# Kernel optimization log

Hardware: AMD Instinct MI355X
Metric: run time of the kernel (lower is better)

The kernel has to match this reference:

```python
import jax
import jax.numpy as jnp
import numpy as np

B, S, D, H, HID, E, TOPK = 1, 2048, 1024, 16, 4096, 8, 2
HEAD_DIM = D // H


def _layer_norm(x, g, b, eps=1e-5):
    mu = jnp.mean(x, axis=-1, keepdims=True)
    var = jnp.var(x, axis=-1, keepdims=True)
    return (x - mu) * jax.lax.rsqrt(var + eps) * g + b


def setup_inputs() -> dict:
    key = jax.random.key(0)
    ks = jax.random.split(key, 12)
    s = 0.02
    return {
        "x": jax.random.normal(ks[0], (B, S, D), jnp.float32),
        "ln1_g": jnp.ones((D,), jnp.float32),
        "ln1_b": jnp.zeros((D,), jnp.float32),
        "wq": jax.random.normal(ks[1], (D, D), jnp.float32) * s,
        "wk": jax.random.normal(ks[2], (D, D), jnp.float32) * s,
        "wv": jax.random.normal(ks[3], (D, D), jnp.float32) * s,
        "wo": jax.random.normal(ks[4], (D, D), jnp.float32) * s,
        "ln2_g": jnp.ones((D,), jnp.float32),
        "ln2_b": jnp.zeros((D,), jnp.float32),
        "w_gate": jax.random.normal(ks[5], (D, E), jnp.float32) * s,
        "w_eg": jax.random.normal(ks[6], (E, D, HID), jnp.float32) * s,
        "w_eu": jax.random.normal(ks[7], (E, D, HID), jnp.float32) * s,
        "w_ed": jax.random.normal(ks[8], (E, HID, D), jnp.float32) * s,
    }


def _attention(h, wq, wk, wv, wo):
    b, s, d = h.shape
    q = (h @ wq).reshape(b, s, H, HEAD_DIM).transpose(0, 2, 1, 3)
    k = (h @ wk).reshape(b, s, H, HEAD_DIM).transpose(0, 2, 1, 3)
    v = (h @ wv).reshape(b, s, H, HEAD_DIM).transpose(0, 2, 1, 3)
    scores = jnp.einsum("bhqd,bhkd->bhqk", q, k) / jnp.sqrt(jnp.asarray(HEAD_DIM, h.dtype))
    causal = jnp.tril(jnp.ones((s, s), bool))  # [s,s]
    scores = jnp.where(causal, scores, jnp.asarray(-1e30, h.dtype))
    attn = jax.nn.softmax(scores, axis=-1)
    out = jnp.einsum("bhqk,bhkd->bhqd", attn, v).transpose(0, 2, 1, 3).reshape(b, s, d)
    return out @ wo


def _moe(h, w_gate, w_eg, w_eu, w_ed):
    b, s, d = h.shape
    flat = h.reshape(-1, d)  # [T,D]
    logits = flat @ w_gate  # [T,E]
    scores = jax.nn.sigmoid(logits)
    top_val, top_idx = jax.lax.top_k(scores, TOPK)
    top_val = top_val / (jnp.sum(top_val, axis=-1, keepdims=True) + 1e-9)
    # per-token per-expert combine weight (0 for unrouted experts)
    combine = jnp.sum(jax.nn.one_hot(top_idx, E, dtype=flat.dtype) * top_val[..., None], axis=1)  # [T,E]
    g = jax.nn.silu(jnp.einsum("td,edh->eth", flat, w_eg))
    u = jnp.einsum("td,edh->eth", flat, w_eu)
    eo = jnp.einsum("eth,ehd->etd", g * u, w_ed)  # [E,T,D]
    out = jnp.einsum("etd,te->td", eo, combine)
    return out.reshape(b, s, d)


def reference(x, ln1_g, ln1_b, wq, wk, wv, wo, ln2_g, ln2_b, w_gate, w_eg, w_eu, w_ed):
    x = x + _attention(_layer_norm(x, ln1_g, ln1_b), wq, wk, wv, wo)
    x = x + _moe(_layer_norm(x, ln2_g, ln2_b), w_gate, w_eg, w_eu, w_ed)
    return x
```

## Files before the change

kernel.cpp:

```cpp
#include <hip/hip_runtime.h>
#include <hip/hip_bf16.h>
#include <stdint.h>

#define DI __device__ __forceinline__

typedef short bf16x8_t __attribute__((ext_vector_type(8)));
typedef float f32x4_t __attribute__((ext_vector_type(4)));

DI unsigned short f2bf(float f) {
  __hip_bfloat16 h = __float2bfloat16(f);
  unsigned short u;
  __builtin_memcpy(&u, &h, 2);
  return u;
}

DI uint32_t pk2(float a, float b) {
  return (uint32_t)f2bf(a) | ((uint32_t)f2bf(b) << 16);
}

DI f32x4_t mfma16(bf16x8_t a, bf16x8_t b, f32x4_t c) {
  return __builtin_amdgcn_mfma_f32_16x16x32_bf16(a, b, c, 0, 0, 0);
}

DI void gload16(const void* g, void* l) {
  __builtin_amdgcn_global_load_lds(
      (const __attribute__((address_space(1))) uint32_t*)g,
      (__attribute__((address_space(3))) uint32_t*)l, 16, 0, 0);
}

DI bf16x8_t frag(const unsigned short* base, int row, int hi) {
  return *(const bf16x8_t*)&base[row * 32 + ((hi ^ ((row >> 1) & 3)) * 8)];
}
DI int chunk_swz(int tid) { return ((tid & 3) ^ ((tid >> 3) & 3)) * 8; }

__global__ __launch_bounds__(256) void transpose_cvt(const float* __restrict__ in,
                                                     unsigned short* __restrict__ out,
                                                     int R, int C) {
  __shared__ float tile[64][65];
  const int tid = threadIdx.x;
  const int tx = tid & 15, ty = tid >> 4;
  const size_t zoff = (size_t)blockIdx.z * R * C;
  const int r0 = blockIdx.y * 64, c0 = blockIdx.x * 64;
#pragma unroll
  for (int i = 0; i < 4; ++i) {
    const int r = ty + i * 16;
    const float4 v = *(const float4*)(in + zoff + (size_t)(r0 + r) * C + c0 + tx * 4);
    tile[r][tx * 4 + 0] = v.x; tile[r][tx * 4 + 1] = v.y;
    tile[r][tx * 4 + 2] = v.z; tile[r][tx * 4 + 3] = v.w;
  }
  __syncthreads();
#pragma unroll
  for (int i = 0; i < 4; ++i) {
    const int r = ty + i * 16;
    ushort4 o;
    o.x = f2bf(tile[tx * 4 + 0][r]); o.y = f2bf(tile[tx * 4 + 1][r]);
    o.z = f2bf(tile[tx * 4 + 2][r]); o.w = f2bf(tile[tx * 4 + 3][r]);
    *(ushort4*)(out + zoff + (size_t)(c0 + r) * R + r0 + tx * 4) = o;
  }
}

__global__ __launch_bounds__(256) void ln_kernel(const float* __restrict__ x, const float* __restrict__ g,
                                                 const float* __restrict__ b, unsigned short* __restrict__ out) {
  const int row = blockIdx.x, tid = threadIdx.x;
  const int wid = tid >> 6, lane = tid & 63;
  const float4 v = *(const float4*)(x + (size_t)row * 1024 + tid * 4);
  float s = v.x + v.y + v.z + v.w;
  float s2 = v.x * v.x + v.y * v.y + v.z * v.z + v.w * v.w;
#pragma unroll
  for (int o = 1; o < 64; o <<= 1) { s += __shfl_xor(s, o); s2 += __shfl_xor(s2, o); }
  __shared__ float red[8];
  if (lane == 0) { red[wid] = s; red[4 + wid] = s2; }
  __syncthreads();
  const float ts = red[0] + red[1] + red[2] + red[3];
  const float ts2 = red[4] + red[5] + red[6] + red[7];
  const float mu = ts * 0.0009765625f;
  const float var = ts2 * 0.0009765625f - mu * mu;
  const float rs = rsqrtf(var + 1e-5f);
  const float4 gg = *(const float4*)(g + tid * 4);
  const float4 bb = *(const float4*)(b + tid * 4);
  ushort4 o4;
  o4.x = f2bf((v.x - mu) * rs * gg.x + bb.x);
  o4.y = f2bf((v.y - mu) * rs * gg.y + bb.y);
  o4.z = f2bf((v.z - mu) * rs * gg.z + bb.z);
  o4.w = f2bf((v.w - mu) * rs * gg.w + bb.w);
  *(ushort4*)(out + (size_t)row * 1024 + tid * 4) = o4;
}

template<int BN>
DI void gemm_loop(const unsigned short* aR0, const unsigned short* aR1,
                  const unsigned short* bR0, const unsigned short* bR1,
                  const int K, unsigned short* lds, const int tid,
                  f32x4_t (&acc)[4][BN / 32]) {
  constexpr int NF = BN / 32;
  unsigned short* ldsA = lds;
  unsigned short* ldsB = lds + 4096;
  const int wid = tid >> 6, lane = tid & 63, ln = lane & 15, hi = lane >> 4;
  const int wr = wid >> 1, wc = wid & 1;
  char* dstA0 = (char*)ldsA + wid * 1024;
  char* dstA1 = (char*)ldsA + 4096 + wid * 1024;
  char* dstB0 = (char*)ldsB + wid * 1024;
  char* dstB1 = (char*)ldsB + 4096 + wid * 1024;
  for (int k0 = 0; k0 < K; k0 += 32) {
    gload16(aR0 + k0, dstA0);
    gload16(aR1 + k0, dstA1);
    gload16(bR0 + k0, dstB0);
    if constexpr (BN == 128) gload16(bR1 + k0, dstB1);
    __syncthreads();
    bf16x8_t af[4];
#pragma unroll
    for (int mf = 0; mf < 4; ++mf)
      af[mf] = frag(ldsA, wr * 64 + mf * 16 + ln, hi);
#pragma unroll
    for (int nf = 0; nf < NF; ++nf) {
      bf16x8_t bfr = frag(ldsB, wc * (BN / 2) + nf * 16 + ln, hi);
#pragma unroll
      for (int mf = 0; mf < 4; ++mf)
        acc[mf][nf] = mfma16(af[mf], bfr, acc[mf][nf]);
    }
    __syncthreads();
  }
}

__global__ __launch_bounds__(256) void qkv_kernel(const unsigned short* __restrict__ h1,
                                                  const unsigned short* __restrict__ wqT,
                                                  const unsigned short* __restrict__ wkT,
                                                  const unsigned short* __restrict__ wvT,
                                                  unsigned short* __restrict__ qb,
                                                  unsigned short* __restrict__ kbf,
                                                  unsigned short* __restrict__ vt) {
  __shared__ unsigned short lds[128 * 32 + 128 * 32];
  const int tid = threadIdx.x;
  const int z = blockIdx.z;
  const unsigned short* BT = (z == 0) ? wqT : (z == 1) ? wkT : wvT;
  const int m0 = blockIdx.y * 128, n0 = blockIdx.x * 128;
  f32x4_t acc[4][4] = {};
  const int cs = chunk_swz(tid);
  const unsigned short* aR0 = h1 + (size_t)(m0 + (tid >> 2)) * 1024 + cs;
  const unsigned short* aR1 = aR0 + 64 * 1024;
  const unsigned short* bR0 = BT + (size_t)(n0 + (tid >> 2)) * 1024 + cs;
  const unsigned short* bR1 = bR0 + 64 * 1024;
  gemm_loop<128>(aR0, aR1, bR0, bR1, 1024, lds, tid, acc);
  const int lane = tid & 63, ln = lane & 15, hi = lane >> 4, wid = tid >> 6;
  const int wr = wid >> 1, wc = wid & 1;
  if (z < 2) {
    unsigned short* o = z ? kbf : qb;
#pragma unroll
    for (int mf = 0; mf < 4; ++mf)
#pragma unroll
      for (int nf = 0; nf < 4; ++nf)
#pragma unroll
        for (int r = 0; r < 4; ++r) {
          const int m = m0 + wr * 64 + mf * 16 + hi * 4 + r;
          const int n = n0 + wc * 64 + nf * 16 + ln;
          o[(size_t)m * 1024 + n] = f2bf(acc[mf][nf][r]);
        }
  } else {
#pragma unroll
    for (int mf = 0; mf < 4; ++mf)
#pragma unroll
      for (int nf = 0; nf < 4; ++nf) {
        const int n = n0 + wc * 64 + nf * 16 + ln;
        const int mb = m0 + wr * 64 + mf * 16 + hi * 4;
        ushort4 o;
        o.x = f2bf(acc[mf][nf][0]); o.y = f2bf(acc[mf][nf][1]);
        o.z = f2bf(acc[mf][nf][2]); o.w = f2bf(acc[mf][nf][3]);
        *(ushort4*)(vt + (size_t)n * 2048 + mb) = o;
      }
  }
}

__global__ __launch_bounds__(256) void wo_kernel(const unsigned short* __restrict__ ao,
                                                 const unsigned short* __restrict__ woT,
                                                 const float* __restrict__ x,
                                                 float* __restrict__ out) {
  __shared__ unsigned short lds[128 * 32 + 64 * 32];
  const int tid = threadIdx.x;
  const int m0 = blockIdx.y * 128, n0 = blockIdx.x * 64;
  f32x4_t acc[4][2] = {};
  const int cs = chunk_swz(tid);
  const unsigned short* aR0 = ao + (size_t)(m0 + (tid >> 2)) * 1024 + cs;
  const unsigned short* aR1 = aR0 + 64 * 1024;
  const unsigned short* bR0 = woT + (size_t)(n0 + (tid >> 2)) * 1024 + cs;
  gemm_loop<64>(aR0, aR1, bR0, nullptr, 1024, lds, tid, acc);
  const int lane = tid & 63, ln = lane & 15, hi = lane >> 4, wid = tid >> 6;
  const int wr = wid >> 1, wc = wid & 1;
#pragma unroll
  for (int mf = 0; mf < 4; ++mf)
#pragma unroll
    for (int nf = 0; nf < 2; ++nf)
#pragma unroll
      for (int r = 0; r < 4; ++r) {
        const int m = m0 + wr * 64 + mf * 16 + hi * 4 + r;
        const int n = n0 + wc * 32 + nf * 16 + ln;
        out[(size_t)m * 1024 + n] = acc[mf][nf][r] + x[(size_t)m * 1024 + n];
      }
}

__global__ __launch_bounds__(256) void attn_kernel(const unsigned short* __restrict__ qb,
                                                   const unsigned short* __restrict__ kbuf,
                                                   const unsigned short* __restrict__ vt,
                                                   unsigned short* __restrict__ ao) {
  __shared__ unsigned short kTl[4096];
  __shared__ unsigned short vTl[4096];
  __shared__ unsigned short pl[4][1024];
  const int tid = threadIdx.x;
  const int wid = tid >> 6, lane = tid & 63;
  const int ln = lane & 15, hi = lane >> 4;
  const int h = blockIdx.y;
  const int q0 = blockIdx.x * 64;
  const int q0w = q0 + wid * 16;

  const unsigned short* qrow = qb + (size_t)(q0w + ln) * 1024 + h * 64 + hi * 8;
  const bf16x8_t aq0 = *(const bf16x8_t*)(qrow);
  const bf16x8_t aq1 = *(const bf16x8_t*)(qrow + 32);

  const int str_r = tid >> 3, str_c = tid & 7;
  const int swc = (str_c ^ (str_r & 7)) * 8;
  const unsigned short* ksrc0 = kbuf + (size_t)str_r * 1024 + h * 64 + swc;
  const unsigned short* ksrc1 = kbuf + (size_t)(str_r + 32) * 1024 + h * 64 + swc;
  const unsigned short* vsrc0 = vt + (size_t)(h * 64 + str_r) * 2048 + swc;
  const unsigned short* vsrc1 = vt + (size_t)(h * 64 + str_r + 32) * 2048 + swc;
  char* kd0 = (char*)kTl + wid * 1024;
  char* kd1 = (char*)kTl + 4096 + wid * 1024;
  char* vd0 = (char*)vTl + wid * 1024;
  char* vd1 = (char*)vTl + 4096 + wid * 1024;

  float m_r[4], l_r[4];
  f32x4_t o_acc[4] = {};
#pragma unroll
  for (int r = 0; r < 4; ++r) { m_r[r] = -1e30f; l_r[r] = 0.f; }

  const int nkv = blockIdx.x + 1;
  for (int it = 0; it < nkv; ++it) {
    const int kv0 = it * 64;
    gload16(ksrc0 + (size_t)kv0 * 1024, kd0);
    gload16(ksrc1 + (size_t)kv0 * 1024, kd1);
    gload16(vsrc0 + kv0, vd0);
    gload16(vsrc1 + kv0, vd1);
    __syncthreads();

    float sc[4][4];
#pragma unroll
    for (int cf = 0; cf < 4; ++cf) {
      const int row = cf * 16 + ln;
      const int swz = row & 7;
      const bf16x8_t b0 = *(const bf16x8_t*)((char*)kTl + row * 128 + ((hi ^ swz) * 16));
      const bf16x8_t b1 = *(const bf16x8_t*)((char*)kTl + row * 128 + (((4 + hi) ^ swz) * 16));
      f32x4_t zacc = {};
      zacc = mfma16(aq0, b0, zacc);
      zacc = mfma16(aq1, b1, zacc);
#pragma unroll
      for (int r = 0; r < 4; ++r) sc[cf][r] = zacc[r] * 0.125f;
    }
    if (kv0 + 63 > q0w) {
#pragma unroll
      for (int cf = 0; cf < 4; ++cf)
#pragma unroll
        for (int r = 0; r < 4; ++r) {
          const int qg = q0w + hi * 4 + r;
          const int kg = kv0 + cf * 16 + ln;
          if (kg > qg) sc[cf][r] = -1e30f;
        }
    }
#pragma unroll
    for (int r = 0; r < 4; ++r) {
      float tm = fmaxf(fmaxf(sc[0][r], sc[1][r]), fmaxf(sc[2][r], sc[3][r]));
      tm = fmaxf(tm, __shfl_xor(tm, 1));
      tm = fmaxf(tm, __shfl_xor(tm, 2));
      tm = fmaxf(tm, __shfl_xor(tm, 4));
      tm = fmaxf(tm, __shfl_xor(tm, 8));
      const float mn = fmaxf(m_r[r], tm);
      const float alpha = __expf(m_r[r] - mn);
      float rsum = 0.f;
#pragma unroll
      for (int cf = 0; cf < 4; ++cf) {
        const float p = __expf(sc[cf][r] - mn);
        sc[cf][r] = p; rsum += p;
      }
      rsum += __shfl_xor(rsum, 1); rsum += __shfl_xor(rsum, 2);
      rsum += __shfl_xor(rsum, 4); rsum += __shfl_xor(rsum, 8);
      l_r[r] = l_r[r] * alpha + rsum;
      m_r[r] = mn;
#pragma unroll
      for (int df = 0; df < 4; ++df) o_acc[df][r] *= alpha;
    }
    unsigned short* pw = &pl[wid][0];
#pragma unroll
    for (int cf = 0; cf < 4; ++cf)
#pragma unroll
      for (int r = 0; r < 4; ++r) {
        const int qq = hi * 4 + r;
        const int kv = cf * 16 + ln;
        const int bo = (qq * 128 + kv * 2) ^ ((qq & 7) << 4);
        *(unsigned short*)((char*)pw + bo) = f2bf(sc[cf][r]);
      }
    __syncthreads();
    const bf16x8_t pa0 = *(const bf16x8_t*)((char*)pw + ((ln * 128 + hi * 16) ^ ((ln & 7) << 4)));
    const bf16x8_t pa1 = *(const bf16x8_t*)((char*)pw + ((ln * 128 + 64 + hi * 16) ^ ((ln & 7) << 4)));
#pragma unroll
    for (int df = 0; df < 4; ++df) {
      const int d = df * 16 + ln;
      const int swz = d & 7;
      const bf16x8_t bv0 = *(const bf16x8_t*)((char*)vTl + d * 128 + ((hi ^ swz) * 16));
      const bf16x8_t bv1 = *(const bf16x8_t*)((char*)vTl + d * 128 + (((4 + hi) ^ swz) * 16));
      o_acc[df] = mfma16(pa0, bv0, o_acc[df]);
      o_acc[df] = mfma16(pa1, bv1, o_acc[df]);
    }
    __syncthreads();
  }
#pragma unroll
  for (int df = 0; df < 4; ++df) {
    const int n = h * 64 + df * 16 + ln;
#pragma unroll
    for (int r = 0; r < 4; ++r) {
      const int m = q0w + hi * 4 + r;
      ao[(size_t)m * 1024 + n] = f2bf(o_acc[df][r] / l_r[r]);
    }
  }
}

__global__ __launch_bounds__(256) void gate_kernel(const float* __restrict__ x2, const float* __restrict__ g,
                                                   const float* __restrict__ b, const float* __restrict__ wg,
                                                   int2* __restrict__ te, float2* __restrict__ tw,
                                                   int* __restrict__ cnt) {
  const int tid = threadIdx.x, wid = tid >> 6, lane = tid & 63;
  const int t = blockIdx.x * 4 + wid;
  const float* row = x2 + (size_t)t * 1024;
  float vv[16];
#pragma unroll
  for (int i = 0; i < 4; ++i) *(float4*)&vv[i * 4] = *(const float4*)(row + lane * 16 + i * 4);
  float s = 0.f, s2 = 0.f;
#pragma unroll
  for (int j = 0; j < 16; ++j) { s += vv[j]; s2 += vv[j] * vv[j]; }
#pragma unroll
  for (int o = 1; o < 64; o <<= 1) { s += __shfl_xor(s, o); s2 += __shfl_xor(s2, o); }
  const float mu = s * 0.0009765625f;
  const float var = s2 * 0.0009765625f - mu * mu;
  const float rs = rsqrtf(var + 1e-5f);
  float acc[8] = {0.f, 0.f, 0.f, 0.f, 0.f, 0.f, 0.f, 0.f};
#pragma unroll
  for (int j = 0; j < 16; ++j) {
    const int d = lane * 16 + j;
    const float xv = (vv[j] - mu) * rs * g[d] + b[d];
    const float4 w0 = *(const float4*)(wg + d * 8);
    const float4 w1 = *(const float4*)(wg + d * 8 + 4);
    acc[0] += xv * w0.x; acc[1] += xv * w0.y; acc[2] += xv * w0.z; acc[3] += xv * w0.w;
    acc[4] += xv * w1.x; acc[5] += xv * w1.y; acc[6] += xv * w1.z; acc[7] += xv * w1.w;
  }
#pragma unroll
  for (int o = 1; o < 64; o <<= 1) {
#pragma unroll
    for (int e = 0; e < 8; ++e) acc[e] += __shfl_xor(acc[e], o);
  }
  if (lane == 0) {
    float sg[8];
#pragma unroll
    for (int e = 0; e < 8; ++e) sg[e] = 1.f / (1.f + __expf(-acc[e]));
    int e0 = 0;
#pragma unroll
    for (int e = 1; e < 8; ++e) if (sg[e] > sg[e0]) e0 = e;
    int e1 = (e0 == 0) ? 1 : 0;
#pragma unroll
    for (int e = 0; e < 8; ++e) if (e != e0 && sg[e] > sg[e1]) e1 = e;
    const float v0 = sg[e0], v1 = sg[e1];
    const float inv = 1.f / (v0 + v1 + 1e-9f);
    te[t] = make_int2(e0, e1);
    tw[t] = make_float2(v0 * inv, v1 * inv);
    atomicAdd(&cnt[e0], 1);
    atomicAdd(&cnt[e1], 1);
  }
}

__global__ void zero_counters(int* p) { if (threadIdx.x < 8) p[threadIdx.x] = 0; }

__global__ void g2_kernel(const int* __restrict__ cnt, int* __restrict__ slot_off,
                          int* __restrict__ tile_expert, int* __restrict__ tile_rowbase,
                          int* __restrict__ cursor, int* __restrict__ assign_token,
                          float* __restrict__ assign_w) {
  const int tid = threadIdx.x;
  for (int i = tid; i < 5120; i += 64) { assign_token[i] = -1; assign_w[i] = 0.f; }
  if (tid == 0) {
    int base = 0, tiles = 0;
    for (int e = 0; e < 8; ++e) {
      const int c = cnt[e];
      slot_off[e] = base;
      cursor[e] = 0;
      const int nt = (c + 127) >> 7;
      for (int i = 0; i < nt; ++i) {
        tile_expert[tiles] = e;
        tile_rowbase[tiles] = base + i * 128;
        ++tiles;
      }
      base += nt * 128;
    }
    for (; tiles < 40; ++tiles) tile_expert[tiles] = -1;
  }
}

__global__ __launch_bounds__(256) void g3_kernel(const int2* __restrict__ te, const float2* __restrict__ tw,
                                                 const int* __restrict__ slot_off, int* __restrict__ cursor,
                                                 int* __restrict__ assign_token, float* __restrict__ assign_w) {
  const int t = blockIdx.x * 256 + threadIdx.x;
  const int2 e = te[t];
  const float2 w = tw[t];
  const int s0 = slot_off[e.x] + atomicAdd(&cursor[e.x], 1);
  assign_token[s0] = t; assign_w[s0] = w.x;
  const int s1 = slot_off[e.y] + atomicAdd(&cursor[e.y], 1);
  assign_token[s1] = t; assign_w[s1] = w.y;
}

__global__ __launch_bounds__(256) void upgate_kernel(const unsigned short* __restrict__ h2,
                                                     const float* __restrict__ w_eg, const float* __restrict__ w_eu,
                                                     const int* __restrict__ tile_expert,
                                                     const int* __restrict__ tile_rowbase,
                                                     const int* __restrict__ assign_token,
                                                     unsigned short* __restrict__ act) {
  const int by = blockIdx.y;
  const int e = tile_expert[by];
  if (e < 0) return;
  const int n0 = blockIdx.x * 64;
  const int rowbase = tile_rowbase[by];
  const int tid = threadIdx.x;
  __shared__ unsigned short lds[128 * 32 + 2 * 64 * 32];
  unsigned short* ldsA = lds;
  unsigned short* ldsB = lds + 4096;
  const int wid = tid >> 6, lane = tid & 63, ln = lane & 15, hi = lane >> 4;
  const int wr = wid >> 1, wc = wid & 1;
  const int r0s = rowbase + (tid >> 2);
  int t0 = assign_token[r0s];       t0 = t0 < 0 ? 0 : t0;
  int t1 = assign_token[r0s + 64];  t1 = t1 < 0 ? 0 : t1;
  const int cs = chunk_swz(tid);
  const unsigned short* aR0 = h2 + (size_t)t0 * 1024 + cs;
  const unsigned short* aR1 = h2 + (size_t)t1 * 1024 + cs;
  char* dstA0 = (char*)ldsA + wid * 1024;
  char* dstA1 = (char*)ldsA + 4096 + wid * 1024;
  const int mat = tid >> 7;
  const int blk = tid & 127;
  const int kb = (blk >> 4) * 4;
  const int nb = (blk & 15) * 4;
  const float* bsrc = (mat ? w_eu : w_eg) + (size_t)e * 1024 * 4096 + (size_t)kb * 4096 + n0 + nb;
  char* bdst[4];
#pragma unroll
  for (int i = 0; i < 4; ++i) {
    const int n = nb + i;
    int bo = mat * 4096 + n * 64 + kb * 2;
    bo ^= ((n >> 2) & 7) << 4;
    bdst[i] = (char*)ldsB + bo;
  }
  f32x4_t accg[4][2] = {};
  f32x4_t accu[4][2] = {};
  for (int k0 = 0; k0 < 1024; k0 += 32) {
    gload16(aR0 + k0, dstA0);
    gload16(aR1 + k0, dstA1);
    const float* bs = bsrc + (size_t)k0 * 4096;
    const float4 q0 = *(const float4*)(bs);
    const float4 q1 = *(const float4*)(bs + 4096);
    const float4 q2 = *(const float4*)(bs + 8192);
    const float4 q3 = *(const float4*)(bs + 12288);
    const float* q0p = (const float*)&q0; const float* q1p = (const float*)&q1;
    const float* q2p = (const float*)&q2; const float* q3p = (const float*)&q3;
#pragma unroll
    for (int i = 0; i < 4; ++i) {
      uint2 w;
      w.x = pk2(q0p[i], q1p[i]);
      w.y = pk2(q2p[i], q3p[i]);
      *(uint2*)bdst[i] = w;
    }
    __syncthreads();
    bf16x8_t af[4];
#pragma unroll
    for (int mf = 0; mf < 4; ++mf)
      af[mf] = frag(ldsA, wr * 64 + mf * 16 + ln, hi);
#pragma unroll
    for (int nf = 0; nf < 2; ++nf) {
      const int nrow = wc * 32 + nf * 16 + ln;
      int bo = nrow * 64 + hi * 16;
      bo ^= ((nrow >> 2) & 7) << 4;
      const bf16x8_t bg = *(const bf16x8_t*)((char*)ldsB + bo);
      const bf16x8_t bu = *(const bf16x8_t*)((char*)ldsB + 4096 + bo);
#pragma unroll
      for (int mf = 0; mf < 4; ++mf) {
        accg[mf][nf] = mfma16(af[mf], bg, accg[mf][nf]);
        accu[mf][nf] = mfma16(af[mf], bu, accu[mf][nf]);
      }
    }
    __syncthreads();
  }
#pragma unroll
  for (int mf = 0; mf < 4; ++mf)
#pragma unroll
    for (int nf = 0; nf < 2; ++nf)
#pragma unroll
      for (int r = 0; r < 4; ++r) {
        const int m = wr * 64 + mf * 16 + hi * 4 + r;
        const int n = n0 + wc * 32 + nf * 16 + ln;
        const float gv = accg[mf][nf][r], uv = accu[mf][nf][r];
        const float val = gv / (1.f + __expf(-gv)) * uv;
        act[(size_t)(rowbase + m) * 4096 + n] = f2bf(val);
      }
}

__global__ __launch_bounds__(256) void down_kernel(const unsigned short* __restrict__ act,
                                                   const float* __restrict__ w_ed,
                                                   const int* __restrict__ tile_expert,
                                                   const int* __restrict__ tile_rowbase,
                                                   const int* __restrict__ assign_token,
                                                   const float* __restrict__ assign_w,
                                                   float* __restrict__ out) {
  const int by = blockIdx.y;
  const int e = tile_expert[by];
  if (e < 0) return;
  const int n0 = blockIdx.x * 64;
  const int rowbase = tile_rowbase[by];
  const int tid = threadIdx.x;
  __shared__ unsigned short lds[128 * 32 + 64 * 32];
  unsigned short* ldsA = lds;
  unsigned short* ldsB = lds + 4096;
  const int wid = tid >> 6, lane = tid & 63, ln = lane & 15, hi = lane >> 4;
  const int wr = wid >> 1, wc = wid & 1;
  const int cs = chunk_swz(tid);
  const unsigned short* aR0 = act + (size_t)(rowbase + (tid >> 2)) * 4096 + cs;
  const unsigned short* aR1 = aR0 + (size_t)64 * 4096;
  char* dstA0 = (char*)ldsA + wid * 1024;
  char* dstA1 = (char*)ldsA + 4096 + wid * 1024;
  const int nb = (tid & 31) * 2;
  const int kb = (tid >> 5) * 4;
  const float* bsrc = w_ed + (size_t)e * 4096 * 1024 + (size_t)kb * 1024 + n0 + nb;
  char* bdst[2];
#pragma unroll
  for (int j = 0; j < 2; ++j) {
    const int n = nb + j;
    int bo = n * 64 + kb * 2;
    bo ^= ((n >> 2) & 7) << 4;
    bdst[j] = (char*)ldsB + bo;
  }
  f32x4_t acc[4][2] = {};
  for (int k0 = 0; k0 < 4096; k0 += 32) {
    gload16(aR0 + k0, dstA0);
    gload16(aR1 + k0, dstA1);
    const float* bs = bsrc + (size_t)k0 * 1024;
    const float2 q0 = *(const float2*)(bs);
    const float2 q1 = *(const float2*)(bs + 1024);
    const float2 q2 = *(const float2*)(bs + 2048);
    const float2 q3 = *(const float2*)(bs + 3072);
    const float* q0p = (const float*)&q0; const float* q1p = (const float*)&q1;
    const float* q2p = (const float*)&q2; const float* q3p = (const float*)&q3;
#pragma unroll
    for (int j = 0; j < 2; ++j) {
      uint2 w;
      w.x = pk2(q0p[j], q1p[j]);
      w.y = pk2(q2p[j], q3p[j]);
      *(uint2*)bdst[j] = w;
    }
    __syncthreads();
    bf16x8_t af[4];
#pragma unroll
    for (int mf = 0; mf < 4; ++mf)
      af[mf] = frag(ldsA, wr * 64 + mf * 16 + ln, hi);
#pragma unroll
    for (int nf = 0; nf < 2; ++nf) {
      const int nrow = wc * 32 + nf * 16 + ln;
      int bo = nrow * 64 + hi * 16;
      bo ^= ((nrow >> 2) & 7) << 4;
      const bf16x8_t bb = *(const bf16x8_t*)((char*)ldsB + bo);
#pragma unroll
      for (int mf = 0; mf < 4; ++mf)
        acc[mf][nf] = mfma16(af[mf], bb, acc[mf][nf]);
    }
    __syncthreads();
  }
#pragma unroll
  for (int mf = 0; mf < 4; ++mf)
#pragma unroll
    for (int r = 0; r < 4; ++r) {
      const int m = wr * 64 + mf * 16 + hi * 4 + r;
      const int slot = rowbase + m;
      const int tk = assign_token[slot];
      if (tk >= 0) {
        const float w = assign_w[slot];
#pragma unroll
        for (int nf = 0; nf < 2; ++nf) {
          const int n = n0 + wc * 32 + nf * 16 + ln;
          atomicAdd(out + (size_t)tk * 1024 + n, acc[mf][nf][r] * w);
        }
      }
    }
}

extern "C" void kernel_launch(void* const* d_in, const int* in_sizes, int n_in,
                              void* d_out, int out_size, void* d_ws, size_t ws_size,
                              hipStream_t stream) {
  (void)in_sizes; (void)n_in; (void)out_size;
  const float* x    = (const float*)d_in[0];
  const float* ln1g = (const float*)d_in[1];
  const float* ln1b = (const float*)d_in[2];
  const float* wq   = (const float*)d_in[3];
  const float* wk   = (const float*)d_in[4];
  const float* wv   = (const float*)d_in[5];
  const float* wo   = (const float*)d_in[6];
  const float* ln2g = (const float*)d_in[7];
  const float* ln2b = (const float*)d_in[8];
  const float* wg   = (const float*)d_in[9];
  const float* weg  = (const float*)d_in[10];
  const float* weu  = (const float*)d_in[11];
  const float* wed  = (const float*)d_in[12];
  float* out = (float*)d_out;
  char* ws = (char*)d_ws;

  const size_t MB = (size_t)1 << 20;
  if (ws_size < 74 * MB) return;
  unsigned short* wqT = (unsigned short*)(ws + 0 * MB);
  unsigned short* wkT = (unsigned short*)(ws + 2 * MB);
  unsigned short* wvT = (unsigned short*)(ws + 4 * MB);
  unsigned short* woT = (unsigned short*)(ws + 6 * MB);
  unsigned short* h1  = (unsigned short*)(ws + 8 * MB);
  unsigned short* qb  = (unsigned short*)(ws + 12 * MB);
  unsigned short* kbf = (unsigned short*)(ws + 16 * MB);
  unsigned short* vt  = (unsigned short*)(ws + 20 * MB);
  unsigned short* ao  = (unsigned short*)(ws + 24 * MB);
  unsigned short* h2  = (unsigned short*)(ws + 28 * MB);
  unsigned short* act = (unsigned short*)(ws + 32 * MB);
  int2*   te = (int2*)(ws + 72 * MB);
  float2* tw = (float2*)(ws + 72 * MB + 16384);
  int*  meta = (int*)(ws + 72 * MB + 32768);
  int* cnt = meta;
  int* cursor = meta + 8;
  int* slot_off = meta + 16;
  int* tile_expert = meta + 24;
  int* tile_rowbase = meta + 64;
  int*   assign_token = (int*)(ws + 72 * MB + 36864);
  float* assign_w     = (float*)(ws + 72 * MB + 36864 + 20480);

  zero_counters<<<1, 64, 0, stream>>>(cnt);
  transpose_cvt<<<dim3(16, 16, 1), 256, 0, stream>>>(wq, wqT, 1024, 1024);
  transpose_cvt<<<dim3(16, 16, 1), 256, 0, stream>>>(wk, wkT, 1024, 1024);
  transpose_cvt<<<dim3(16, 16, 1), 256, 0, stream>>>(wv, wvT, 1024, 1024);
  transpose_cvt<<<dim3(16, 16, 1), 256, 0, stream>>>(wo, woT, 1024, 1024);
  ln_kernel<<<2048, 256, 0, stream>>>(x, ln1g, ln1b, h1);
  qkv_kernel<<<dim3(8, 16, 3), 256, 0, stream>>>(h1, wqT, wkT, wvT, qb, kbf, vt);
  attn_kernel<<<dim3(32, 16), 256, 0, stream>>>(qb, kbf, vt, ao);
  wo_kernel<<<dim3(16, 16), 256, 0, stream>>>(ao, woT, x, out);
  ln_kernel<<<2048, 256, 0, stream>>>(out, ln2g, ln2b, h2);
  gate_kernel<<<512, 256, 0, stream>>>(out, ln2g, ln2b, wg, te, tw, cnt);
  g2_kernel<<<1, 64, 0, stream>>>(cnt, slot_off, tile_expert, tile_rowbase, cursor, assign_token, assign_w);
  g3_kernel<<<8, 256, 0, stream>>>(te, tw, slot_off, cursor, assign_token, assign_w);
  upgate_kernel<<<dim3(64, 40), 256, 0, stream>>>(h2, weg, weu, tile_expert, tile_rowbase, assign_token, act);
  down_kernel<<<dim3(16, 40), 256, 0, stream>>>(act, wed, tile_expert, tile_rowbase, assign_token, assign_w, out);
}
```

Measured before the change: 508.2 us.

## Double-buffer LDS in MoE up-gate and down kernels to prefetch next K tile

Converts the expert up/gate and down GEMM K-loops to double-buffered LDS. The next tile's activation and fp32 weight loads are issued before the current tile's MFMAs, so global latency overlaps compute, and only one barrier remains per iteration. The down kernel also remaps its weight loads to float4 per thread. In exchange, LDS use per block doubles and register pressure rises from holding prefetched values, which can lower occupancy.

```diff
diff --git a/kernel.cpp b/kernel.cpp
--- a/kernel.cpp
+++ b/kernel.cpp
@@ -421,9 +421,9 @@
   const int n0 = blockIdx.x * 64;
   const int rowbase = tile_rowbase[by];
   const int tid = threadIdx.x;
-  __shared__ unsigned short lds[128 * 32 + 2 * 64 * 32];
+  __shared__ unsigned short lds[2 * 4096 + 2 * 4096];
   unsigned short* ldsA = lds;
-  unsigned short* ldsB = lds + 4096;
+  unsigned short* ldsB = lds + 8192;
   const int wid = tid >> 6, lane = tid & 63, ln = lane & 15, hi = lane >> 4;
   const int wr = wid >> 1, wc = wid & 1;
   const int r0s = rowbase + (tid >> 2);
@@ -432,31 +432,28 @@
   const int cs = chunk_swz(tid);
   const unsigned short* aR0 = h2 + (size_t)t0 * 1024 + cs;
   const unsigned short* aR1 = h2 + (size_t)t1 * 1024 + cs;
-  char* dstA0 = (char*)ldsA + wid * 1024;
-  char* dstA1 = (char*)ldsA + 4096 + wid * 1024;
   const int mat = tid >> 7;
   const int blk = tid & 127;
   const int kb = (blk >> 4) * 4;
   const int nb = (blk & 15) * 4;
   const float* bsrc = (mat ? w_eu : w_eg) + (size_t)e * 1024 * 4096 + (size_t)kb * 4096 + n0 + nb;
-  char* bdst[4];
+  int boff[4];
 #pragma unroll
   for (int i = 0; i < 4; ++i) {
     const int n = nb + i;
     int bo = mat * 4096 + n * 64 + kb * 2;
     bo ^= ((n >> 2) & 7) << 4;
-    bdst[i] = (char*)ldsB + bo;
+    boff[i] = bo;
   }
   f32x4_t accg[4][2] = {};
   f32x4_t accu[4][2] = {};
-  for (int k0 = 0; k0 < 1024; k0 += 32) {
-    gload16(aR0 + k0, dstA0);
-    gload16(aR1 + k0, dstA1);
-    const float* bs = bsrc + (size_t)k0 * 4096;
-    const float4 q0 = *(const float4*)(bs);
-    const float4 q1 = *(const float4*)(bs + 4096);
-    const float4 q2 = *(const float4*)(bs + 8192);
-    const float4 q3 = *(const float4*)(bs + 12288);
+  gload16(aR0, (char*)ldsA + wid * 1024);
+  gload16(aR1, (char*)ldsA + 4096 + wid * 1024);
+  {
+    const float4 q0 = *(const float4*)(bsrc);
+    const float4 q1 = *(const float4*)(bsrc + 4096);
+    const float4 q2 = *(const float4*)(bsrc + 8192);
+    const float4 q3 = *(const float4*)(bsrc + 12288);
     const float* q0p = (const float*)&q0; const float* q1p = (const float*)&q1;
     const float* q2p = (const float*)&q2; const float* q3p = (const float*)&q3;
 #pragma unroll
@@ -464,27 +461,58 @@
       uint2 w;
       w.x = pk2(q0p[i], q1p[i]);
       w.y = pk2(q2p[i], q3p[i]);
-      *(uint2*)bdst[i] = w;
-    }
-    __syncthreads();
+      *(uint2*)((char*)ldsB + boff[i]) = w;
+    }
+  }
+  __syncthreads();
+  int buf = 0;
+  for (int k0 = 0; k0 < 1024; k0 += 32) {
+    const int kn = k0 + 32;
+    const int nbuf = buf ^ 1;
+    const bool pf = kn < 1024;
+    float4 q0, q1, q2, q3;
+    if (pf) {
+      gload16(aR0 + kn, (char*)ldsA + nbuf * 8192 + wid * 1024);
+      gload16(aR1 + kn, (char*)ldsA + nbuf * 8192 + 4096 + wid * 1024);
+      const float* bs = bsrc + (size_t)kn * 4096;
+      q0 = *(const float4*)(bs);
+      q1 = *(const float4*)(bs + 4096);
+      q2 = *(const float4*)(bs + 8192);
+      q3 = *(const float4*)(bs + 12288);
+    }
+    const unsigned short* A = ldsA + buf * 4096;
+    const char* Bb = (char*)ldsB + buf * 8192;
     bf16x8_t af[4];
 #pragma unroll
     for (int mf = 0; mf < 4; ++mf)
-      af[mf] = frag(ldsA, wr * 64 + mf * 16 + ln, hi);
+      af[mf] = frag(A, wr * 64 + mf * 16 + ln, hi);
 #pragma unroll
     for (int nf = 0; nf < 2; ++nf) {
       const int nrow = wc * 32 + nf * 16 + ln;
       int bo = nrow * 64 + hi * 16;
       bo ^= ((nrow >> 2) & 7) << 4;
-      const bf16x8_t bg = *(const bf16x8_t*)((char*)ldsB + bo);
-      const bf16x8_t bu = *(const bf16x8_t*)((char*)ldsB + 4096 + bo);
+      const bf16x8_t bg = *(const bf16x8_t*)(Bb + bo);
+      const bf16x8_t bu = *(const bf16x8_t*)(Bb + 4096 + bo);
 #pragma unroll
       for (int mf = 0; mf < 4; ++mf) {
         accg[mf][nf] = mfma16(af[mf], bg, accg[mf][nf]);
         accu[mf][nf] = mfma16(af[mf], bu, accu[mf][nf]);
       }
     }
+    if (pf) {
+      char* Bn = (char*)ldsB + nbuf * 8192;
+      const float* q0p = (const float*)&q0; const float* q1p = (const float*)&q1;
+      const float* q2p = (const float*)&q2; const float* q3p = (const float*)&q3;
+#pragma unroll
+      for (int i = 0; i < 4; ++i) {
+        uint2 w;
+        w.x = pk2(q0p[i], q1p[i]);
+        w.y = pk2(q2p[i], q3p[i]);
+        *(uint2*)(Bn + boff[i]) = w;
+      }
+    }
     __syncthreads();
+    buf = nbuf;
   }
 #pragma unroll
   for (int mf = 0; mf < 4; ++mf)
@@ -513,61 +541,75 @@
   const int n0 = blockIdx.x * 64;
   const int rowbase = tile_rowbase[by];
   const int tid = threadIdx.x;
-  __shared__ unsigned short lds[128 * 32 + 64 * 32];
+  __shared__ unsigned short lds[2 * 4096 + 2 * 2048];
   unsigned short* ldsA = lds;
-  unsigned short* ldsB = lds + 4096;
+  unsigned short* ldsB = lds + 8192;
   const int wid = tid >> 6, lane = tid & 63, ln = lane & 15, hi = lane >> 4;
   const int wr = wid >> 1, wc = wid & 1;
   const int cs = chunk_swz(tid);
   const unsigned short* aR0 = act + (size_t)(rowbase + (tid >> 2)) * 4096 + cs;
   const unsigned short* aR1 = aR0 + (size_t)64 * 4096;
-  char* dstA0 = (char*)ldsA + wid * 1024;
-  char* dstA1 = (char*)ldsA + 4096 + wid * 1024;
-  const int nb = (tid & 31) * 2;
-  const int kb = (tid >> 5) * 4;
-  const float* bsrc = w_ed + (size_t)e * 4096 * 1024 + (size_t)kb * 1024 + n0 + nb;
-  char* bdst[2];
-#pragma unroll
-  for (int j = 0; j < 2; ++j) {
-    const int n = nb + j;
-    int bo = n * 64 + kb * 2;
+  const int nb = (tid & 15) * 4;
+  const int kb2 = (tid >> 4) * 2;
+  const float* bsrc = w_ed + (size_t)e * 4096 * 1024 + (size_t)kb2 * 1024 + n0 + nb;
+  int boff[4];
+#pragma unroll
+  for (int i = 0; i < 4; ++i) {
+    const int n = nb + i;
+    int bo = n * 64 + kb2 * 2;
     bo ^= ((n >> 2) & 7) << 4;
-    bdst[j] = (char*)ldsB + bo;
+    boff[i] = bo;
   }
   f32x4_t acc[4][2] = {};
+  gload16(aR0, (char*)ldsA + wid * 1024);
+  gload16(aR1, (char*)ldsA + 4096 + wid * 1024);
+  {
+    const float4 q0 = *(const float4*)(bsrc);
+    const float4 q1 = *(const float4*)(bsrc + 1024);
+    const float* q0p = (const float*)&q0; const float* q1p = (const float*)&q1;
+#pragma unroll
+    for (int i = 0; i < 4; ++i)
+      *(uint32_t*)((char*)ldsB + boff[i]) = pk2(q0p[i], q1p[i]);
+  }
+  __syncthreads();
+  int buf = 0;
   for (int k0 = 0; k0 < 4096; k0 += 32) {
-    gload16(aR0 + k0, dstA0);
-    gload16(aR1 + k0, dstA1);
-    const float* bs = bsrc + (size_t)k0 * 1024;
-    const float2 q0 = *(const float2*)(bs);
-    const float2 q1 = *(const float2*)(bs + 1024);
-    const float2 q2 = *(const float2*)(bs + 2048);
-    const float2 q3 = *(const float2*)(bs + 3072);
-    const float* q0p = (const float*)&q0; const float* q1p = (const float*)&q1;
-    const float* q2p = (const float*)&q2; const float* q3p = (const float*)&q3;
-#pragma unroll
-    for (int j = 0; j < 2; ++j) {
-      uint2 w;
-      w.x = pk2(q0p[j], q1p[j]);
-      w.y = pk2(q2p[j], q3p[j]);
-      *(uint2*)bdst[j] = w;
-    }
-    __syncthreads();
+    const int kn = k0 + 32;
+    const int nbuf = buf ^ 1;
+    const bool pf = kn < 4096;
+    float4 q0, q1;
+    if (pf) {
+      gload16(aR0 + kn, (char*)ldsA + nbuf * 8192 + wid * 1024);
+      gload16(aR1 + kn, (char*)ldsA + nbuf * 8192 + 4096 + wid * 1024);
+      const float* bs = bsrc + (size_t)kn * 1024;
+      q0 = *(const float4*)(bs);
+      q1 = *(const float4*)(bs + 1024);
+    }
+    const unsigned short* A = ldsA + buf * 4096;
+    const char* Bb = (char*)ldsB + buf * 4096;
     bf16x8_t af[4];
 #pragma unroll
     for (int mf = 0; mf < 4; ++mf)
-      af[mf] = frag(ldsA, wr * 64 + mf * 16 + ln, hi);
+      af[mf] = frag(A, wr * 64 + mf * 16 + ln, hi);
 #pragma unroll
     for (int nf = 0; nf < 2; ++nf) {
       const int nrow = wc * 32 + nf * 16 + ln;
       int bo = nrow * 64 + hi * 16;
       bo ^= ((nrow >> 2) & 7) << 4;
-      const bf16x8_t bb = *(const bf16x8_t*)((char*)ldsB + bo);
+      const bf16x8_t bb = *(const bf16x8_t*)(Bb + bo);
 #pragma unroll
       for (int mf = 0; mf < 4; ++mf)
         acc[mf][nf] = mfma16(af[mf], bb, acc[mf][nf]);
     }
+    if (pf) {
+      char* Bn = (char*)ldsB + nbuf * 4096;
+      const float* q0p = (const float*)&q0; const float* q1p = (const float*)&q1;
+#pragma unroll
+      for (int i = 0; i < 4; ++i)
+        *(uint32_t*)(Bn + boff[i]) = pk2(q0p[i], q1p[i]);
+    }
     __syncthreads();
+    buf = nbuf;
   }
 #pragma unroll
   for (int mf = 0; mf < 4; ++mf)
```

Result: slower. 525.6 us (+3.4%).

## Double waves per MoE GEMM block and split down-projection K four ways

Applied to the files above, without the earlier changes.

The up/gate and down expert GEMM kernels now run 512 threads per block. Each of the eight waves computes a 64x16 slice instead of a 64x32 slice, and each thread loads one A row and two B k-rows per step. The down projection is split along K into four z-slices of 1024, which gives four times as many blocks to fill the GPU and shortens each block's serial K loop. The cost is four times as many fp32 atomicAdds into the output and a larger workspace requirement, moved from 74 to 86 MB, where the launcher silently does nothing if the buffer is too small.

```diff
diff --git a/kernel.cpp b/kernel.cpp
--- a/kernel.cpp
+++ b/kernel.cpp
@@ -373,12 +373,12 @@
 
 __global__ void zero_counters(int* p) { if (threadIdx.x < 8) p[threadIdx.x] = 0; }
 
-__global__ void g2_kernel(const int* __restrict__ cnt, int* __restrict__ slot_off,
-                          int* __restrict__ tile_expert, int* __restrict__ tile_rowbase,
-                          int* __restrict__ cursor, int* __restrict__ assign_token,
-                          float* __restrict__ assign_w) {
+__global__ __launch_bounds__(256) void g2_kernel(const int* __restrict__ cnt, int* __restrict__ slot_off,
+                                                 int* __restrict__ tile_expert, int* __restrict__ tile_rowbase,
+                                                 int* __restrict__ cursor, int* __restrict__ assign_token,
+                                                 float* __restrict__ assign_w) {
   const int tid = threadIdx.x;
-  for (int i = tid; i < 5120; i += 64) { assign_token[i] = -1; assign_w[i] = 0.f; }
+  for (int i = tid; i < 5120; i += 256) { assign_token[i] = -1; assign_w[i] = 0.f; }
   if (tid == 0) {
     int base = 0, tiles = 0;
     for (int e = 0; e < 8; ++e) {
@@ -409,7 +409,7 @@
   assign_token[s1] = t; assign_w[s1] = w.y;
 }
 
-__global__ __launch_bounds__(256) void upgate_kernel(const unsigned short* __restrict__ h2,
+__global__ __launch_bounds__(512) void upgate_kernel(const unsigned short* __restrict__ h2,
                                                      const float* __restrict__ w_eg, const float* __restrict__ w_eu,
                                                      const int* __restrict__ tile_expert,
                                                      const int* __restrict__ tile_rowbase,
@@ -425,82 +425,68 @@
   unsigned short* ldsA = lds;
   unsigned short* ldsB = lds + 4096;
   const int wid = tid >> 6, lane = tid & 63, ln = lane & 15, hi = lane >> 4;
-  const int wr = wid >> 1, wc = wid & 1;
-  const int r0s = rowbase + (tid >> 2);
-  int t0 = assign_token[r0s];       t0 = t0 < 0 ? 0 : t0;
-  int t1 = assign_token[r0s + 64];  t1 = t1 < 0 ? 0 : t1;
-  const int cs = chunk_swz(tid);
-  const unsigned short* aR0 = h2 + (size_t)t0 * 1024 + cs;
-  const unsigned short* aR1 = h2 + (size_t)t1 * 1024 + cs;
-  char* dstA0 = (char*)ldsA + wid * 1024;
-  char* dstA1 = (char*)ldsA + 4096 + wid * 1024;
-  const int mat = tid >> 7;
-  const int blk = tid & 127;
-  const int kb = (blk >> 4) * 4;
+  const int wr = wid >> 2, wc = wid & 3;
+  int tk = assign_token[rowbase + (tid >> 2)];
+  tk = tk < 0 ? 0 : tk;
+  const unsigned short* aR = h2 + (size_t)tk * 1024 + chunk_swz(tid);
+  char* dstA = (char*)ldsA + wid * 1024;
+  const int mat = tid >> 8;
+  const int blk = tid & 255;
+  const int kb = (blk >> 4) * 2;
   const int nb = (blk & 15) * 4;
   const float* bsrc = (mat ? w_eu : w_eg) + (size_t)e * 1024 * 4096 + (size_t)kb * 4096 + n0 + nb;
-  char* bdst[4];
+  int boff[4];
 #pragma unroll
   for (int i = 0; i < 4; ++i) {
     const int n = nb + i;
     int bo = mat * 4096 + n * 64 + kb * 2;
     bo ^= ((n >> 2) & 7) << 4;
-    bdst[i] = (char*)ldsB + bo;
-  }
-  f32x4_t accg[4][2] = {};
-  f32x4_t accu[4][2] = {};
+    boff[i] = bo;
+  }
+  f32x4_t accg[4];
+  f32x4_t accu[4];
+#pragma unroll
+  for (int i = 0; i < 4; ++i) { accg[i] = (f32x4_t){0,0,0,0}; accu[i] = (f32x4_t){0,0,0,0}; }
   for (int k0 = 0; k0 < 1024; k0 += 32) {
-    gload16(aR0 + k0, dstA0);
-    gload16(aR1 + k0, dstA1);
+    gload16(aR + k0, dstA);
     const float* bs = bsrc + (size_t)k0 * 4096;
     const float4 q0 = *(const float4*)(bs);
     const float4 q1 = *(const float4*)(bs + 4096);
-    const float4 q2 = *(const float4*)(bs + 8192);
-    const float4 q3 = *(const float4*)(bs + 12288);
-    const float* q0p = (const float*)&q0; const float* q1p = (const float*)&q1;
-    const float* q2p = (const float*)&q2; const float* q3p = (const float*)&q3;
-#pragma unroll
-    for (int i = 0; i < 4; ++i) {
-      uint2 w;
-      w.x = pk2(q0p[i], q1p[i]);
-      w.y = pk2(q2p[i], q3p[i]);
-      *(uint2*)bdst[i] = w;
-    }
+    const float* q0p = (const float*)&q0;
+    const float* q1p = (const float*)&q1;
+#pragma unroll
+    for (int i = 0; i < 4; ++i)
+      *(uint32_t*)((char*)ldsB + boff[i]) = pk2(q0p[i], q1p[i]);
     __syncthreads();
     bf16x8_t af[4];
 #pragma unroll
     for (int mf = 0; mf < 4; ++mf)
       af[mf] = frag(ldsA, wr * 64 + mf * 16 + ln, hi);
-#pragma unroll
-    for (int nf = 0; nf < 2; ++nf) {
-      const int nrow = wc * 32 + nf * 16 + ln;
-      int bo = nrow * 64 + hi * 16;
-      bo ^= ((nrow >> 2) & 7) << 4;
-      const bf16x8_t bg = *(const bf16x8_t*)((char*)ldsB + bo);
-      const bf16x8_t bu = *(const bf16x8_t*)((char*)ldsB + 4096 + bo);
-#pragma unroll
-      for (int mf = 0; mf < 4; ++mf) {
-        accg[mf][nf] = mfma16(af[mf], bg, accg[mf][nf]);
-        accu[mf][nf] = mfma16(af[mf], bu, accu[mf][nf]);
-      }
-    }
-    __syncthreads();
-  }
+    const int nrow = wc * 16 + ln;
+    int bo = nrow * 64 + hi * 16;
+    bo ^= ((nrow >> 2) & 7) << 4;
+    const bf16x8_t bg = *(const bf16x8_t*)((char*)ldsB + bo);
+    const bf16x8_t bu = *(const bf16x8_t*)((char*)ldsB + 4096 + bo);
+#pragma unroll
+    for (int mf = 0; mf < 4; ++mf) {
+      accg[mf] = mfma16(af[mf], bg, accg[mf]);
+      accu[mf] = mfma16(af[mf], bu, accu[mf]);
+    }
+    __syncthreads();
+  }
+  const int n = n0 + wc * 16 + ln;
 #pragma unroll
   for (int mf = 0; mf < 4; ++mf)
 #pragma unroll
-    for (int nf = 0; nf < 2; ++nf)
-#pragma unroll
-      for (int r = 0; r < 4; ++r) {
-        const int m = wr * 64 + mf * 16 + hi * 4 + r;
-        const int n = n0 + wc * 32 + nf * 16 + ln;
-        const float gv = accg[mf][nf][r], uv = accu[mf][nf][r];
-        const float val = gv / (1.f + __expf(-gv)) * uv;
-        act[(size_t)(rowbase + m) * 4096 + n] = f2bf(val);
-      }
-}
-
-__global__ __launch_bounds__(256) void down_kernel(const unsigned short* __restrict__ act,
+    for (int r = 0; r < 4; ++r) {
+      const int m = wr * 64 + mf * 16 + hi * 4 + r;
+      const float gv = accg[mf][r], uv = accu[mf][r];
+      const float val = gv / (1.f + __expf(-gv)) * uv;
+      act[(size_t)(rowbase + m) * 4096 + n] = f2bf(val);
+    }
+}
+
+__global__ __launch_bounds__(512) void down_kernel(const unsigned short* __restrict__ act,
                                                    const float* __restrict__ w_ed,
                                                    const int* __restrict__ tile_expert,
                                                    const int* __restrict__ tile_rowbase,
@@ -510,65 +496,56 @@
   const int by = blockIdx.y;
   const int e = tile_expert[by];
   if (e < 0) return;
+  const int rowbase = tile_rowbase[by];
   const int n0 = blockIdx.x * 64;
-  const int rowbase = tile_rowbase[by];
+  const int kz = blockIdx.z * 1024;
   const int tid = threadIdx.x;
   __shared__ unsigned short lds[128 * 32 + 64 * 32];
   unsigned short* ldsA = lds;
   unsigned short* ldsB = lds + 4096;
   const int wid = tid >> 6, lane = tid & 63, ln = lane & 15, hi = lane >> 4;
-  const int wr = wid >> 1, wc = wid & 1;
-  const int cs = chunk_swz(tid);
-  const unsigned short* aR0 = act + (size_t)(rowbase + (tid >> 2)) * 4096 + cs;
-  const unsigned short* aR1 = aR0 + (size_t)64 * 4096;
-  char* dstA0 = (char*)ldsA + wid * 1024;
-  char* dstA1 = (char*)ldsA + 4096 + wid * 1024;
+  const int wr = wid >> 2, wc = wid & 3;
+  const unsigned short* aR = act + (size_t)(rowbase + (tid >> 2)) * 4096 + kz + chunk_swz(tid);
+  char* dstA = (char*)ldsA + wid * 1024;
   const int nb = (tid & 31) * 2;
-  const int kb = (tid >> 5) * 4;
-  const float* bsrc = w_ed + (size_t)e * 4096 * 1024 + (size_t)kb * 1024 + n0 + nb;
-  char* bdst[2];
+  const int kb = (tid >> 5) * 2;
+  const float* bsrc = w_ed + (size_t)e * 4096 * 1024 + (size_t)(kz + kb) * 1024 + n0 + nb;
+  int boff[2];
 #pragma unroll
   for (int j = 0; j < 2; ++j) {
     const int n = nb + j;
     int bo = n * 64 + kb * 2;
     bo ^= ((n >> 2) & 7) << 4;
-    bdst[j] = (char*)ldsB + bo;
-  }
-  f32x4_t acc[4][2] = {};
-  for (int k0 = 0; k0 < 4096; k0 += 32) {
-    gload16(aR0 + k0, dstA0);
-    gload16(aR1 + k0, dstA1);
+    boff[j] = bo;
+  }
+  f32x4_t acc[4];
+#pragma unroll
+  for (int i = 0; i < 4; ++i) acc[i] = (f32x4_t){0,0,0,0};
+  for (int k0 = 0; k0 < 1024; k0 += 32) {
+    gload16(aR + k0, dstA);
     const float* bs = bsrc + (size_t)k0 * 1024;
     const float2 q0 = *(const float2*)(bs);
     const float2 q1 = *(const float2*)(bs + 1024);
-    const float2 q2 = *(const float2*)(bs + 2048);
-    const float2 q3 = *(const float2*)(bs + 3072);
-    const float* q0p = (const float*)&q0; const float* q1p = (const float*)&q1;
-    const float* q2p = (const float*)&q2; const float* q3p = (const float*)&q3;
-#pragma unroll
-    for (int j = 0; j < 2; ++j) {
-      uint2 w;
-      w.x = pk2(q0p[j], q1p[j]);
-      w.y = pk2(q2p[j], q3p[j]);
-      *(uint2*)bdst[j] = w;
-    }
+    const float* q0p = (const float*)&q0;
+    const float* q1p = (const float*)&q1;
+#pragma unroll
+    for (int j = 0; j < 2; ++j)
+      *(uint32_t*)((char*)ldsB + boff[j]) = pk2(q0p[j], q1p[j]);
     __syncthreads();
     bf16x8_t af[4];
 #pragma unroll
     for (int mf = 0; mf < 4; ++mf)
       af[mf] = frag(ldsA, wr * 64 + mf * 16 + ln, hi);
-#pragma unroll
-    for (int nf = 0; nf < 2; ++nf) {
-      const int nrow = wc * 32 + nf * 16 + ln;
-      int bo = nrow * 64 + hi * 16;
-      bo ^= ((nrow >> 2) & 7) << 4;
-      const bf16x8_t bb = *(const bf16x8_t*)((char*)ldsB + bo);
-#pragma unroll
-      for (int mf = 0; mf < 4; ++mf)
-        acc[mf][nf] = mfma16(af[mf], bb, acc[mf][nf]);
-    }
-    __syncthreads();
-  }
+    const int nrow = wc * 16 + ln;
+    int bo = nrow * 64 + hi * 16;
+    bo ^= ((nrow >> 2) & 7) << 4;
+    const bf16x8_t bb = *(const bf16x8_t*)((char*)ldsB + bo);
+#pragma unroll
+    for (int mf = 0; mf < 4; ++mf)
+      acc[mf] = mfma16(af[mf], bb, acc[mf]);
+    __syncthreads();
+  }
+  const int n = n0 + wc * 16 + ln;
 #pragma unroll
   for (int mf = 0; mf < 4; ++mf)
 #pragma unroll
@@ -578,11 +555,7 @@
       const int tk = assign_token[slot];
       if (tk >= 0) {
         const float w = assign_w[slot];
-#pragma unroll
-        for (int nf = 0; nf < 2; ++nf) {
-          const int n = n0 + wc * 32 + nf * 16 + ln;
-          atomicAdd(out + (size_t)tk * 1024 + n, acc[mf][nf][r] * w);
-        }
+        atomicAdd(out + (size_t)tk * 1024 + n, acc[mf][r] * w);
       }
     }
 }
@@ -608,7 +581,7 @@
   char* ws = (char*)d_ws;
 
   const size_t MB = (size_t)1 << 20;
-  if (ws_size < 74 * MB) return;
+  if (ws_size < 86 * MB) return;
   unsigned short* wqT = (unsigned short*)(ws + 0 * MB);
   unsigned short* wkT = (unsigned short*)(ws + 2 * MB);
   unsigned short* wvT = (unsigned short*)(ws + 4 * MB);
@@ -620,16 +593,16 @@
   unsigned short* ao  = (unsigned short*)(ws + 24 * MB);
   unsigned short* h2  = (unsigned short*)(ws + 28 * MB);
   unsigned short* act = (unsigned short*)(ws + 32 * MB);
-  int2*   te = (int2*)(ws + 72 * MB);
-  float2* tw = (float2*)(ws + 72 * MB + 16384);
-  int*  meta = (int*)(ws + 72 * MB + 32768);
+  int2*   te = (int2*)(ws + 84 * MB);
+  float2* tw = (float2*)(ws + 84 * MB + 16384);
+  int*  meta = (int*)(ws + 84 * MB + 32768);
   int* cnt = meta;
   int* cursor = meta + 8;
   int* slot_off = meta + 16;
   int* tile_expert = meta + 24;
   int* tile_rowbase = meta + 64;
-  int*   assign_token = (int*)(ws + 72 * MB + 36864);
-  float* assign_w     = (float*)(ws + 72 * MB + 36864 + 20480);
+  int*   assign_token = (int*)(ws + 84 * MB + 36864);
+  float* assign_w     = (float*)(ws + 84 * MB + 36864 + 32768);
 
   zero_counters<<<1, 64, 0, stream>>>(cnt);
   transpose_cvt<<<dim3(16, 16, 1), 256, 0, stream>>>(wq, wqT, 1024, 1024);
@@ -642,8 +615,8 @@
   wo_kernel<<<dim3(16, 16), 256, 0, stream>>>(ao, woT, x, out);
   ln_kernel<<<2048, 256, 0, stream>>>(out, ln2g, ln2b, h2);
   gate_kernel<<<512, 256, 0, stream>>>(out, ln2g, ln2b, wg, te, tw, cnt);
-  g2_kernel<<<1, 64, 0, stream>>>(cnt, slot_off, tile_expert, tile_rowbase, cursor, assign_token, assign_w);
+  g2_kernel<<<1, 256, 0, stream>>>(cnt, slot_off, tile_expert, tile_rowbase, cursor, assign_token, assign_w);
   g3_kernel<<<8, 256, 0, stream>>>(te, tw, slot_off, cursor, assign_token, assign_w);
-  upgate_kernel<<<dim3(64, 40), 256, 0, stream>>>(h2, weg, weu, tile_expert, tile_rowbase, assign_token, act);
-  down_kernel<<<dim3(16, 40), 256, 0, stream>>>(act, wed, tile_expert, tile_rowbase, assign_token, assign_w, out);
-}
+  upgate_kernel<<<dim3(64, 40), 512, 0, stream>>>(h2, weg, weu, tile_expert, tile_rowbase, assign_token, act);
+  down_kernel<<<dim3(16, 40, 4), 512, 0, stream>>>(act, wed, tile_expert, tile_rowbase, assign_token, assign_w, out);
+}
```

After: 547.3 us. 7.7% more time.
